# Optimization experiments

Measured on AMD Instinct MI355X. Metric: run time of the kernel, lower is better.

Reference implementation:

```python
import jax, jax.numpy as jnp
import numpy as np

# Module constants (from init_kwargs)
DILATION = (1, 1)
KERNEL = (3, 3)
PADDING = (1, 1)
STRIDE = (1, 1)
IN_SHAPE = (4, 64, 224, 224)  # b, c, ih, iw


def _build_indices():
    b, c, ih, iw = IN_SHAPE
    ih += 2 * PADDING[0]
    iw += 2 * PADDING[1]
    nh = KERNEL[0] + DILATION[0]
    nw = KERNEL[1] + DILATION[1]
    idx1 = np.array([
        list(range(i * DILATION[0], ih - nh + i * DILATION[0] + 1, STRIDE[0]))
        for i in range(KERNEL[0])
    ], dtype=np.int32)  # [kh, oh]
    idx2 = np.array([
        list(range(j * DILATION[1], iw - nw + j * DILATION[1] + 1, STRIDE[1]))
        for j in range(KERNEL[1])
    ], dtype=np.int32)  # [kw, ow]
    return idx1, idx2


def setup_inputs() -> dict:
    key = jax.random.key(0)
    x = jax.random.normal(key, IN_SHAPE, dtype=jnp.float32)
    return {"x": x}


def reference(x):
    b, c, _, _ = IN_SHAPE
    kh, kw = KERNEL
    idx1, idx2 = _build_indices()  # static numpy index grids
    # pad H and W
    xp = jnp.pad(x, ((0, 0), (0, 0), (PADDING[0], PADDING[0]), (PADDING[1], PADDING[1])))
    # gather rows: [b, c, kh, oh, iw_p]
    v1 = xp[:, :, idx1, :]
    # gather cols: [b, c, kh, oh, kw, ow]
    v2 = v1[:, :, :, :, idx2]
    # permute to [b, c, kh, kw, oh, ow] then flatten to [b, c*kh*kw, oh*ow]
    v3 = jnp.transpose(v2, (0, 1, 2, 4, 3, 5))
    return v3.reshape(b, c * kh * kw, -1)
```

## Files before the change

### kernel.cpp

```cpp
#include <hip/hip_runtime.h>


#define TOTAL_ELEMS 114575616u
#define N_VEC4      28643904u
#define PLANE_IN    50176u

__global__ __launch_bounds__(256) void unfold223_kernel(
    const float* __restrict__ x, float* __restrict__ out)
{
    unsigned int t = blockIdx.x * 256u + threadIdx.x;
    if (t >= N_VEC4) return;
    unsigned int n = t * 4u;

    unsigned int ch  = n / 49729u;
    unsigned int pos = n - ch * 49729u;
    unsigned int oh  = pos / 223u;
    unsigned int ow  = pos - oh * 223u;
    unsigned int q   = ch / 9u;
    unsigned int r   = ch - q * 9u;
    unsigned int i   = r / 3u;
    unsigned int j   = r - i * 3u;

    float v[4];
#pragma unroll
    for (int e = 0; e < 4; ++e) {
        int ih = (int)(oh + i) - 1;
        int iw = (int)(ow + j) - 1;
        bool valid = ((unsigned)ih < 224u) && ((unsigned)iw < 224u);
        unsigned int cih = valid ? (unsigned)ih : 0u;
        unsigned int ciw = valid ? (unsigned)iw : 0u;
        float val = x[q * PLANE_IN + cih * 224u + ciw];
        v[e] = valid ? val : 0.0f;

        ow++;
        if (ow == 223u) {
            ow = 0u; oh++;
            if (oh == 223u) {
                oh = 0u; j++;
                if (j == 3u) {
                    j = 0u; i++;
                    if (i == 3u) { i = 0u; q++; }
                }
            }
        }
    }

    reinterpret_cast<float4*>(out)[t] = make_float4(v[0], v[1], v[2], v[3]);
}

extern "C" void kernel_launch(void* const* d_in, const int* in_sizes, int n_in,
                              void* d_out, int out_size, void* d_ws, size_t ws_size,
                              hipStream_t stream)
{
    const float* x = (const float*)d_in[0];
    float* out = (float*)d_out;
    unsigned int blocks = (N_VEC4 + 255u) / 256u;
    unfold223_kernel<<<dim3(blocks), dim3(256), 0, stream>>>(x, out);
}
```

Measured before the change: 547.6 us.

## Compute all nine kernel offsets per thread from shared row loads

Each thread now owns four output columns of one output row in one input channel. It loads three input rows once as vector loads and writes all nine shifted (kh,kw) output planes, instead of each thread gathering four scalars for a single flattened output position. This removes the per-element div/mod index math and the repeated scalar gathers of the same input values. The cost is unaligned vector loads and stores, and edge-case logic for the first column, the first row and the overlapping last column chunk (col 219), which may write some values twice. The kernel also assumes the sizes used in this workload.

```diff
diff --git a/kernel.cpp b/kernel.cpp
--- a/kernel.cpp
+++ b/kernel.cpp
@@ -1,51 +1,65 @@
 #include <hip/hip_runtime.h>
 
 
-#define TOTAL_ELEMS 114575616u
-#define N_VEC4      28643904u
-#define PLANE_IN    50176u
+#define OW       223u
+#define OSP      49729ull
+#define IW       224u
+#define PLANE_IN 50176u
 
-__global__ __launch_bounds__(256) void unfold223_kernel(
+typedef float vf4 __attribute__((ext_vector_type(4)));
+typedef vf4 vf4u __attribute__((aligned(4)));
+
+__global__ __launch_bounds__(448) void unfold223_v7(
     const float* __restrict__ x, float* __restrict__ out)
 {
-    unsigned int t = blockIdx.x * 256u + threadIdx.x;
-    if (t >= N_VEC4) return;
-    unsigned int n = t * 4u;
+    const unsigned q    = blockIdx.y;
+    const unsigned band = blockIdx.x;
+    const unsigned t    = threadIdx.x;
+    const unsigned rr   = t / 56u;
+    const unsigned k    = t - rr * 56u;
+    const unsigned r    = band * 8u + rr;
+    if (r > 222u) return;
 
-    unsigned int ch  = n / 49729u;
-    unsigned int pos = n - ch * 49729u;
-    unsigned int oh  = pos / 223u;
-    unsigned int ow  = pos - oh * 223u;
-    unsigned int q   = ch / 9u;
-    unsigned int r   = ch - q * 9u;
-    unsigned int i   = r / 3u;
-    unsigned int j   = r - i * 3u;
+    const unsigned col0  = (k == 55u) ? 219u : 4u * k;
+    const bool     edge0 = (col0 == 0u);
+    const unsigned co    = edge0 ? 0u : col0 - 1u;
+    const unsigned rm    = (r == 0u) ? 0u : r - 1u;
 
-    float v[4];
-#pragma unroll
-    for (int e = 0; e < 4; ++e) {
-        int ih = (int)(oh + i) - 1;
-        int iw = (int)(ow + j) - 1;
-        bool valid = ((unsigned)ih < 224u) && ((unsigned)iw < 224u);
-        unsigned int cih = valid ? (unsigned)ih : 0u;
-        unsigned int ciw = valid ? (unsigned)iw : 0u;
-        float val = x[q * PLANE_IN + cih * 224u + ciw];
-        v[e] = valid ? val : 0.0f;
+    const float* __restrict__ xq = x + q * PLANE_IN;
 
-        ow++;
-        if (ow == 223u) {
-            ow = 0u; oh++;
-            if (oh == 223u) {
-                oh = 0u; j++;
-                if (j == 3u) {
-                    j = 0u; i++;
-                    if (i == 3u) { i = 0u; q++; }
-                }
-            }
-        }
+    const vf4 am = *reinterpret_cast<const vf4u*>(xq + rm * IW + co);
+    const vf4 bm = *reinterpret_cast<const vf4u*>(xq + rm * IW + col0 + 1u);
+    const vf4 a0 = *reinterpret_cast<const vf4u*>(xq + r  * IW + co);
+    const vf4 b0 = *reinterpret_cast<const vf4u*>(xq + r  * IW + col0 + 1u);
+    const vf4 ap = *reinterpret_cast<const vf4u*>(xq + (r + 1u) * IW + co);
+    const vf4 bp = *reinterpret_cast<const vf4u*>(xq + (r + 1u) * IW + col0 + 1u);
+
+#define TRIO(a, b, q0, q1, q2)                                     \
+    vf4 q0, q1, q2;                                                \
+    if (edge0) { q0 = (vf4){0.0f, a.x, a.y, a.z}; q1 = a; }        \
+    else       { q0 = a; q1 = (vf4){a.y, a.z, a.w, b.z}; }         \
+    q2 = b;
+
+    TRIO(am, bm, t00, t01, t02)
+    TRIO(a0, b0, t10, t11, t12)
+    TRIO(ap, bp, t20, t21, t22)
+
+    if (r == 0u) {
+        t00 = (vf4)0.0f; t01 = (vf4)0.0f; t02 = (vf4)0.0f;
     }
 
-    reinterpret_cast<float4*>(out)[t] = make_float4(v[0], v[1], v[2], v[3]);
+    float* __restrict__ och = out + (unsigned long long)q * 9ull * OSP;
+    const unsigned rc = r * OW + col0;
+
+    *reinterpret_cast<vf4u*>(och + 0ull * OSP + rc) = t00;
+    *reinterpret_cast<vf4u*>(och + 1ull * OSP + rc) = t01;
+    *reinterpret_cast<vf4u*>(och + 2ull * OSP + rc) = t02;
+    *reinterpret_cast<vf4u*>(och + 3ull * OSP + rc) = t10;
+    *reinterpret_cast<vf4u*>(och + 4ull * OSP + rc) = t11;
+    *reinterpret_cast<vf4u*>(och + 5ull * OSP + rc) = t12;
+    *reinterpret_cast<vf4u*>(och + 6ull * OSP + rc) = t20;
+    *reinterpret_cast<vf4u*>(och + 7ull * OSP + rc) = t21;
+    *reinterpret_cast<vf4u*>(och + 8ull * OSP + rc) = t22;
 }
 
 extern "C" void kernel_launch(void* const* d_in, const int* in_sizes, int n_in,
@@ -54,6 +68,5 @@
 {
     const float* x = (const float*)d_in[0];
     float* out = (float*)d_out;
-    unsigned int blocks = (N_VEC4 + 255u) / 256u;
-    unfold223_kernel<<<dim3(blocks), dim3(256), 0, stream>>>(x, out);
+    unfold223_v7<<<dim3(28, 256), dim3(448), 0, stream>>>(x, out);
 }
```

Result: faster. 499.2 us (-8.8%).
